# Kernel tuning notes

Hardware: AMD Instinct MI355X
Metric: run time of the kernel (lower is better)

## Reference

```python
import jax, jax.numpy as jnp
import numpy as np
import math

WINDOW = 2048
EMBED = 1024
BATCH = 8


def setup_inputs() -> dict:
    key = jax.random.key(0)
    ks = jax.random.split(key, 7)
    s = 1.0 / math.sqrt(EMBED)
    return {
        "embeddings": jax.random.normal(ks[0], (BATCH, WINDOW, EMBED), dtype=jnp.float32),
        "Wq": jax.random.uniform(ks[1], (EMBED, EMBED), jnp.float32, -s, s),
        "bq": jax.random.uniform(ks[2], (EMBED,), jnp.float32, -s, s),
        "Wk": jax.random.uniform(ks[3], (EMBED, EMBED), jnp.float32, -s, s),
        "bk": jax.random.uniform(ks[4], (EMBED,), jnp.float32, -s, s),
        "Wv": jax.random.uniform(ks[5], (EMBED, EMBED), jnp.float32, -s, s),
        "bv": jax.random.uniform(ks[6], (EMBED,), jnp.float32, -s, s),
    }


def reference(embeddings, Wq, bq, Wk, bk, Wv, bv):
    # Linear layers: x @ W.T + b (torch nn.Linear convention)
    Q = jnp.einsum('bse,fe->bsf', embeddings, Wq) + bq
    K = jnp.einsum('bse,fe->bsf', embeddings, Wk) + bk
    V = jnp.einsum('bse,fe->bsf', embeddings, Wv) + bv
    scale = 1.0 / math.sqrt(EMBED)
    # [B, S, S] score matrix: A[b, i, j] = Q_i . K_j / sqrt(d)
    A = jnp.einsum('bie,bje->bij', Q, K) * scale
    # causal additive mask: -inf where j > i (strictly upper triangular)
    mask = jnp.triu(jnp.full((WINDOW, WINDOW), -jnp.inf, dtype=A.dtype), k=1)
    A = A + mask
    # NOTE: faithful to original nn.Softmax(dim=1): normalize over QUERY axis
    P = jax.nn.softmax(A, axis=1)
    return jnp.einsum('bij,bje->bie', P, V)
```

## Files before the change

### kernel.cpp

```cpp
#include <hip/hip_runtime.h>
#include <stdint.h>

#define WINDOW 2048
#define EMBED  1024
#define BATCH  8
#define MTOT   (BATCH*WINDOW)

typedef unsigned short u16;
typedef __bf16 bf16x8 __attribute__((ext_vector_type(8)));
typedef float  f32x4  __attribute__((ext_vector_type(4)));

#define BK 64
#define KSCALE 0.04508422717564447f

#define BM2 256
#define BN2 256
#define HALF2 8192
#define PLD  260

#define AHALFR 4096
#define BHALFR 8192

#define WAITVM4 asm volatile("s_waitcnt vmcnt(4)" ::: "memory")
#define WAITVM3 asm volatile("s_waitcnt vmcnt(3)" ::: "memory")
#define WAITVM0 asm volatile("s_waitcnt vmcnt(0)" ::: "memory")
#define SBAR    __builtin_amdgcn_s_barrier()

__device__ __forceinline__ u16 f2bf(float f) {
  union { float f; unsigned u; } a; a.f = f;
  unsigned r = a.u + 0x7FFF + ((a.u >> 16) & 1);
  return (u16)(r >> 16);
}
__device__ __forceinline__ float bf2f(u16 u) {
  union { unsigned u; float f; } a; a.u = ((unsigned)u) << 16;
  return a.f;
}

__device__ __forceinline__ void gload16(const u16* g, u16* l) {
  __builtin_amdgcn_global_load_lds(
      (const __attribute__((address_space(1))) unsigned int*)g,
      (__attribute__((address_space(3))) unsigned int*)l, 16, 0, 0);
}


__device__ __forceinline__ void gemm256(
    const u16* __restrict__ A, int lda,
    const u16* __restrict__ B, int ldb,
    int nt, u16* lds, f32x4 acc[8][4])
{
  const int tid  = threadIdx.x;
  const int lane = tid & 63;
  const int wid  = tid >> 6;
  const int wm   = (wid >> 2) * 128;
  const int wn   = (wid & 3) * 64;
  const int lrow = lane & 15;
  const int hi   = lane >> 4;
  u16* dA = lds;
  u16* dB = lds + 4 * HALF2;

  int aoff[8], boff[4];
  #pragma unroll
  for (int mi = 0; mi < 8; ++mi) {
    int r = wm + mi * 16 + lrow;
    aoff[mi] = r * 32 + ((hi ^ ((r >> 1) & 3)) << 3);
  }
  #pragma unroll
  for (int ni = 0; ni < 4; ++ni) {
    int r = wn + ni * 16 + lrow;
    boff[ni] = r * 32 + ((hi ^ ((r >> 1) & 3)) << 3);
  }

  const int f0 = tid, f1 = 512 + tid;
  const int r0 = f0 >> 2, r1 = f1 >> 2;
  const int c0 = (((f0 & 3) ^ ((r0 >> 1) & 3)) << 3);
  const int c1 = (((f1 & 3) ^ ((r1 >> 1) & 3)) << 3);
  const u16* pA0 = A + (size_t)r0 * lda + c0;
  const u16* pA1 = A + (size_t)r1 * lda + c1;
  const u16* pB0 = B + (size_t)r0 * ldb + c0;
  const u16* pB1 = B + (size_t)r1 * ldb + c1;
  const int d0 = f0 * 8, d1 = f1 * 8;

  gload16(pA0,      dA + d0);         gload16(pA1,      dA + d1);
  gload16(pB0,      dB + d0);         gload16(pB1,      dB + d1);
  gload16(pA0 + 32, dA + HALF2 + d0); gload16(pA1 + 32, dA + HALF2 + d1);
  gload16(pB0 + 32, dB + HALF2 + d0); gload16(pB1 + 32, dB + HALF2 + d1);
  pA0 += BK; pA1 += BK; pB0 += BK; pB1 += BK;
  WAITVM4;
  SBAR;

  for (int t = 0; t < nt; ++t) {
    const int cb = (t & 1) * 2;
    const int nb = ((t + 1) & 1) * 2;
    u16* LA0 = dA + cb * HALF2;  u16* LA1 = LA0 + HALF2;
    u16* LB0 = dB + cb * HALF2;  u16* LB1 = LB0 + HALF2;
    const bool s = (t + 1) < nt;
    bf16x8 av[8], bv[4];

    #pragma unroll
    for (int mi = 0; mi < 8; ++mi) av[mi] = *(const bf16x8*)(LA0 + aoff[mi]);
    #pragma unroll
    for (int ni = 0; ni < 4; ++ni) bv[ni] = *(const bf16x8*)(LB0 + boff[ni]);
    if (s) {
      gload16(pA0, dA + nb * HALF2 + d0); gload16(pA1, dA + nb * HALF2 + d1);
      gload16(pB0, dB + nb * HALF2 + d0); gload16(pB1, dB + nb * HALF2 + d1);
    }
    __builtin_amdgcn_s_setprio(1);
    #pragma unroll
    for (int mi = 0; mi < 8; ++mi)
      #pragma unroll
      for (int ni = 0; ni < 4; ++ni)
        acc[mi][ni] = __builtin_amdgcn_mfma_f32_16x16x32_bf16(av[mi], bv[ni], acc[mi][ni], 0, 0, 0);
    __builtin_amdgcn_s_setprio(0);
    if (s) { WAITVM4; } else { WAITVM0; }
    SBAR;

    #pragma unroll
    for (int mi = 0; mi < 8; ++mi) av[mi] = *(const bf16x8*)(LA1 + aoff[mi]);
    #pragma unroll
    for (int ni = 0; ni < 4; ++ni) bv[ni] = *(const bf16x8*)(LB1 + boff[ni]);
    if (s) {
      gload16(pA0 + 32, dA + nb * HALF2 + HALF2 + d0); gload16(pA1 + 32, dA + nb * HALF2 + HALF2 + d1);
      gload16(pB0 + 32, dB + nb * HALF2 + HALF2 + d0); gload16(pB1 + 32, dB + nb * HALF2 + HALF2 + d1);
      pA0 += BK; pA1 += BK; pB0 += BK; pB1 += BK;
    }
    __builtin_amdgcn_s_setprio(1);
    #pragma unroll
    for (int mi = 0; mi < 8; ++mi)
      #pragma unroll
      for (int ni = 0; ni < 4; ++ni)
        acc[mi][ni] = __builtin_amdgcn_mfma_f32_16x16x32_bf16(av[mi], bv[ni], acc[mi][ni], 0, 0, 0);
    __builtin_amdgcn_s_setprio(0);
    if (s) { WAITVM4; }
    SBAR;
  }
}

__device__ __forceinline__ void gemm_rect(
    const u16* __restrict__ A, int lda,
    const u16* __restrict__ B, int ldb,
    int nt, u16* lds, f32x4 acc[4][4])
{
  const int tid  = threadIdx.x;
  const int lane = tid & 63;
  const int wid  = tid >> 6;
  const int wm   = (wid >> 2) * 64;
  const int wn   = (wid & 3) * 64;
  const int lrow = lane & 15;
  const int hi   = lane >> 4;
  u16* dA = lds;
  u16* dB = lds + 4 * AHALFR;

  int aoff[4], boff[4];
  #pragma unroll
  for (int mi = 0; mi < 4; ++mi) {
    int r = wm + mi * 16 + lrow;
    aoff[mi] = r * 32 + ((hi ^ ((r >> 1) & 3)) << 3);
  }
  #pragma unroll
  for (int ni = 0; ni < 4; ++ni) {
    int r = wn + ni * 16 + lrow;
    boff[ni] = r * 32 + ((hi ^ ((r >> 1) & 3)) << 3);
  }

  const int fa = tid;
  const int fb0 = tid, fb1 = 512 + tid;
  const int ra = fa >> 2, rb0 = fb0 >> 2, rb1 = fb1 >> 2;
  const int ca  = (((fa  & 3) ^ ((ra  >> 1) & 3)) << 3);
  const int cb0 = (((fb0 & 3) ^ ((rb0 >> 1) & 3)) << 3);
  const int cb1 = (((fb1 & 3) ^ ((rb1 >> 1) & 3)) << 3);
  const u16* pA  = A + (size_t)ra  * lda + ca;
  const u16* pB0 = B + (size_t)rb0 * ldb + cb0;
  const u16* pB1 = B + (size_t)rb1 * ldb + cb1;
  const int da = fa * 8, db0 = fb0 * 8, db1 = fb1 * 8;

  gload16(pA,       dA + da);
  gload16(pB0,      dB + db0);          gload16(pB1,      dB + db1);
  gload16(pA + 32,  dA + AHALFR + da);
  gload16(pB0 + 32, dB + BHALFR + db0); gload16(pB1 + 32, dB + BHALFR + db1);
  pA += BK; pB0 += BK; pB1 += BK;
  WAITVM3;
  SBAR;

  for (int t = 0; t < nt; ++t) {
    const int cb = (t & 1) * 2;
    const int nb = ((t + 1) & 1) * 2;
    u16* LA0 = dA + cb * AHALFR;  u16* LA1 = LA0 + AHALFR;
    u16* LB0 = dB + cb * BHALFR;  u16* LB1 = LB0 + BHALFR;
    const bool s = (t + 1) < nt;
    bf16x8 av[4], bv[4];

    #pragma unroll
    for (int mi = 0; mi < 4; ++mi) av[mi] = *(const bf16x8*)(LA0 + aoff[mi]);
    #pragma unroll
    for (int ni = 0; ni < 4; ++ni) bv[ni] = *(const bf16x8*)(LB0 + boff[ni]);
    if (s) {
      gload16(pA,  dA + nb * AHALFR + da);
      gload16(pB0, dB + nb * BHALFR + db0); gload16(pB1, dB + nb * BHALFR + db1);
    }
    __builtin_amdgcn_s_setprio(1);
    #pragma unroll
    for (int mi = 0; mi < 4; ++mi)
      #pragma unroll
      for (int ni = 0; ni < 4; ++ni)
        acc[mi][ni] = __builtin_amdgcn_mfma_f32_16x16x32_bf16(av[mi], bv[ni], acc[mi][ni], 0, 0, 0);
    __builtin_amdgcn_s_setprio(0);
    if (s) { WAITVM3; } else { WAITVM0; }
    SBAR;

    #pragma unroll
    for (int mi = 0; mi < 4; ++mi) av[mi] = *(const bf16x8*)(LA1 + aoff[mi]);
    #pragma unroll
    for (int ni = 0; ni < 4; ++ni) bv[ni] = *(const bf16x8*)(LB1 + boff[ni]);
    if (s) {
      gload16(pA + 32,  dA + nb * AHALFR + AHALFR + da);
      gload16(pB0 + 32, dB + nb * BHALFR + BHALFR + db0);
      gload16(pB1 + 32, dB + nb * BHALFR + BHALFR + db1);
      pA += BK; pB0 += BK; pB1 += BK;
    }
    __builtin_amdgcn_s_setprio(1);
    #pragma unroll
    for (int mi = 0; mi < 4; ++mi)
      #pragma unroll
      for (int ni = 0; ni < 4; ++ni)
        acc[mi][ni] = __builtin_amdgcn_mfma_f32_16x16x32_bf16(av[mi], bv[ni], acc[mi][ni], 0, 0, 0);
    __builtin_amdgcn_s_setprio(0);
    if (s) { WAITVM3; }
    SBAR;
  }
}

__global__ __launch_bounds__(256) void k_cvt(const float* __restrict__ in,
                                             u16* __restrict__ out, int n) {
  int i = (blockIdx.x * 256 + threadIdx.x) * 4;
  if (i >= n) return;
  float4 v = *(const float4*)(in + i);
  ushort4 o;
  o.x = f2bf(v.x); o.y = f2bf(v.y); o.z = f2bf(v.z); o.w = f2bf(v.w);
  *(ushort4*)(out + i) = o;
}

__global__ __launch_bounds__(256) void k_cvtw(const float* __restrict__ w0,
                                              const float* __restrict__ w1,
                                              const float* __restrict__ w2,
                                              u16* __restrict__ out) {
  const float* in = (blockIdx.y == 0) ? w0 : (blockIdx.y == 1) ? w1 : w2;
  u16* o = out + (size_t)blockIdx.y * EMBED * EMBED;
  int i = (blockIdx.x * 256 + threadIdx.x) * 4;
  float4 v = *(const float4*)(in + i);
  ushort4 r;
  r.x = f2bf(v.x); r.y = f2bf(v.y); r.z = f2bf(v.z); r.w = f2bf(v.w);
  *(ushort4*)(o + i) = r;
}

__global__ __launch_bounds__(512, 2) void k_qkv(
    const u16* __restrict__ Xb, const u16* __restrict__ Wb,
    const float* __restrict__ bq, const float* __restrict__ bk, const float* __restrict__ bv,
    u16* __restrict__ Q, u16* __restrict__ Ks, u16* __restrict__ V)
{
  __shared__ u16 lds[8 * HALF2];
  const int m0 = blockIdx.x * BM2;
  const int n0 = blockIdx.y * BN2;
  const int z  = blockIdx.z;
  const u16*   W    = Wb + (size_t)z * EMBED * EMBED;
  const float* bias = (z == 0) ? bq : (z == 1) ? bk : bv;
  u16* out          = (z == 0) ? Q  : (z == 1) ? Ks : V;
  const float scale = (z == 1) ? KSCALE : 1.0f;

  f32x4 acc[8][4];
  const f32x4 zz = {0.f,0.f,0.f,0.f};
  #pragma unroll
  for (int i = 0; i < 8; ++i) for (int j = 0; j < 4; ++j) acc[i][j] = zz;
  gemm256(Xb + (size_t)m0 * EMBED, EMBED, W + (size_t)n0 * EMBED, EMBED,
          EMBED / BK, lds, acc);

  const int lane = threadIdx.x & 63, wid = threadIdx.x >> 6;
  const int wm = (wid >> 2) * 128, wn = (wid & 3) * 64;
  const int lrow = lane & 15, hi = lane >> 4;
  #pragma unroll
  for (int mi = 0; mi < 8; ++mi)
    #pragma unroll
    for (int ni = 0; ni < 4; ++ni)
      #pragma unroll
      for (int rr = 0; rr < 4; ++rr) {
        int gm = m0 + wm + mi * 16 + hi * 4 + rr;
        int gn = n0 + wn + ni * 16 + lrow;
        out[(size_t)gm * EMBED + gn] = f2bf((acc[mi][ni][rr] + bias[gn]) * scale);
      }
}

__global__ __launch_bounds__(512, 2) void k_spd(
    const u16* __restrict__ Q, const u16* __restrict__ Ks,
    u16* __restrict__ P, float* __restrict__ D)
{
  __shared__ u16 lds[BM2 * PLD];
  const int sblk = blockIdx.x;

  if (sblk < 256) {
    const int xcd = sblk & 7;
    const int q   = sblk >> 3;
    int it = 0;
    while (q >= ((it + 1) * (it + 2)) / 2) ++it;
    const int jt = q - (it * (it + 1)) / 2;
    const int b  = (xcd - it) & 7;
    const int i0 = it * BM2;
    const int j0 = jt * BN2;

    const u16* A = Q  + (size_t)b * WINDOW * EMBED + (size_t)i0 * EMBED;
    const u16* B = Ks + (size_t)b * WINDOW * EMBED + (size_t)j0 * EMBED;
    f32x4 acc[8][4];
    const f32x4 zz = {0.f,0.f,0.f,0.f};
    #pragma unroll
    for (int i = 0; i < 8; ++i) for (int j = 0; j < 4; ++j) acc[i][j] = zz;
    gemm256(A, EMBED, B, EMBED, EMBED / BK, lds, acc);

    u16* Pb   = P + (size_t)b * WINDOW * WINDOW;
    float* Db = D + (size_t)b * WINDOW;
    const int tid  = threadIdx.x;
    const int lane = tid & 63, wid = tid >> 6;
    const int wm = (wid >> 2) * 128, wn = (wid & 3) * 64;
    const int lrow = lane & 15, hi = lane >> 4;

    #pragma unroll
    for (int ni = 0; ni < 4; ++ni) {
      int lj = wn + ni * 16 + lrow;
      float csum = 0.f;
      #pragma unroll
      for (int mi = 0; mi < 8; ++mi)
        #pragma unroll
        for (int rr = 0; rr < 4; ++rr) {
          int li = wm + mi * 16 + hi * 4 + rr;
          float p = ((i0 + li) >= (j0 + lj)) ? exp2f(acc[mi][ni][rr]) : 0.0f;
          lds[li * PLD + lj] = f2bf(p);
          csum += p;
        }
      csum += __shfl_xor(csum, 16, 64);
      csum += __shfl_xor(csum, 32, 64);
      if (hi == 0) atomicAdd(&Db[j0 + lj], csum);
    }
    __syncthreads();

    #pragma unroll
    for (int it2 = 0; it2 < 16; ++it2) {
      int f   = it2 * 512 + tid;
      int row = f >> 5;
      int c   = f & 31;
      bf16x8 v = *(const bf16x8*)(lds + row * PLD + c * 8);
      *(bf16x8*)(Pb + (size_t)(i0 + row) * WINDOW + j0 + c * 8) = v;
    }
  } else {
    const int ih   = sblk - 256;
    const int xcd  = ih & 7;
    const int h    = ih >> 3;
    const int jt   = 4 + (h >> 1);
    const int half = h & 1;
    const int it   = 7;
    const int b    = (xcd - it) & 7;
    const int i0   = it * BM2 + half * 128;
    const int j0   = jt * BN2;

    const u16* A = Q  + (size_t)b * WINDOW * EMBED + (size_t)i0 * EMBED;
    const u16* B = Ks + (size_t)b * WINDOW * EMBED + (size_t)j0 * EMBED;
    f32x4 acc[4][4];
    const f32x4 zz = {0.f,0.f,0.f,0.f};
    #pragma unroll
    for (int i = 0; i < 4; ++i) for (int j = 0; j < 4; ++j) acc[i][j] = zz;
    gemm_rect(A, EMBED, B, EMBED, EMBED / BK, lds, acc);

    u16* Pb   = P + (size_t)b * WINDOW * WINDOW;
    float* Db = D + (size_t)b * WINDOW;
    const int lane = threadIdx.x & 63, wid = threadIdx.x >> 6;
    const int wm = (wid >> 2) * 64, wn = (wid & 3) * 64;
    const int lrow = lane & 15, hi = lane >> 4;
    #pragma unroll
    for (int ni = 0; ni < 4; ++ni) {
      int gj = j0 + wn + ni * 16 + lrow;
      float csum = 0.f;
      #pragma unroll
      for (int mi = 0; mi < 4; ++mi)
        #pragma unroll
        for (int rr = 0; rr < 4; ++rr) {
          int gi = i0 + wm + mi * 16 + hi * 4 + rr;
          float p = (gi >= gj) ? exp2f(acc[mi][ni][rr]) : 0.0f;
          Pb[(size_t)gi * WINDOW + gj] = f2bf(p);
          csum += p;
        }
      csum += __shfl_xor(csum, 16, 64);
      csum += __shfl_xor(csum, 32, 64);
      if (hi == 0) atomicAdd(&Db[gj], csum);
    }
  }
}

__global__ __launch_bounds__(256) void k_vdt(
    const u16* __restrict__ V, const float* __restrict__ D, u16* __restrict__ Vdt)
{
  __shared__ u16 tile[64][68];
  const int j0 = blockIdx.x * 64, e0 = blockIdx.y * 64, b = blockIdx.z;
  const u16* Vb = V   + (size_t)b * WINDOW * EMBED;
  u16* Tb       = Vdt + (size_t)b * EMBED * WINDOW;
  const float* Db = D + (size_t)b * WINDOW;
  const int t = threadIdx.x;
  const int rr = t >> 4;
  const int cc = (t & 15) * 4;
  #pragma unroll
  for (int p = 0; p < 4; ++p) {
    int r = p * 16 + rr;
    *(uint2*)&tile[r][cc] = *(const uint2*)(Vb + (size_t)(j0 + r) * EMBED + e0 + cc);
  }
  __syncthreads();
  #pragma unroll
  for (int p = 0; p < 4; ++p) {
    int er = p * 16 + rr;
    ushort4 o;
    o.x = f2bf(bf2f(tile[cc + 0][er]) / Db[j0 + cc + 0]);
    o.y = f2bf(bf2f(tile[cc + 1][er]) / Db[j0 + cc + 1]);
    o.z = f2bf(bf2f(tile[cc + 2][er]) / Db[j0 + cc + 2]);
    o.w = f2bf(bf2f(tile[cc + 3][er]) / Db[j0 + cc + 3]);
    *(ushort4*)(Tb + (size_t)(e0 + er) * WINDOW + j0 + cc) = o;
  }
}

__global__ __launch_bounds__(512, 2) void k_out(
    const u16* __restrict__ P, const u16* __restrict__ Vdt, float* __restrict__ O)
{
  __shared__ u16 lds[8 * HALF2];
  const int s   = blockIdx.x;
  const int xcd = s & 7;
  const int q   = s >> 3;
  const int et  = q & 3;
  const int it  = 7 - (q >> 2);
  const int b   = (xcd - it) & 7;
  const int i0  = it * BM2;
  const int e0  = et * BN2;

  const u16* A = P   + (size_t)b * WINDOW * WINDOW + (size_t)i0 * WINDOW;
  const u16* B = Vdt + (size_t)b * EMBED * WINDOW  + (size_t)e0 * WINDOW;
  f32x4 acc[8][4];
  const f32x4 zz = {0.f,0.f,0.f,0.f};
  #pragma unroll
  for (int i = 0; i < 8; ++i) for (int j = 0; j < 4; ++j) acc[i][j] = zz;
  gemm256(A, WINDOW, B, WINDOW, (i0 + BM2) / BK, lds, acc);

  float* Ob = O + (size_t)b * WINDOW * EMBED;
  const int lane = threadIdx.x & 63, wid = threadIdx.x >> 6;
  const int wm = (wid >> 2) * 128, wn = (wid & 3) * 64;
  const int lrow = lane & 15, hi = lane >> 4;
  #pragma unroll
  for (int mi = 0; mi < 8; ++mi)
    #pragma unroll
    for (int ni = 0; ni < 4; ++ni)
      #pragma unroll
      for (int rr = 0; rr < 4; ++rr) {
        int gi = i0 + wm + mi * 16 + hi * 4 + rr;
        int ge = e0 + wn + ni * 16 + lrow;
        Ob[(size_t)gi * EMBED + ge] = acc[mi][ni][rr];
      }
}

extern "C" void kernel_launch(void* const* d_in, const int* in_sizes, int n_in,
                              void* d_out, int out_size, void* d_ws, size_t ws_size,
                              hipStream_t stream) {
  const float* X  = (const float*)d_in[0];
  const float* Wq = (const float*)d_in[1];
  const float* bq = (const float*)d_in[2];
  const float* Wk = (const float*)d_in[3];
  const float* bk = (const float*)d_in[4];
  const float* Wv = (const float*)d_in[5];
  const float* bv = (const float*)d_in[6];
  float* O = (float*)d_out;

  char* ws = (char*)d_ws;
  size_t off = 0;
  auto alloc = [&](size_t bytes) -> void* {
    void* p = ws + off; off += (bytes + 255) & ~(size_t)255; return p;
  };
  u16*  Xb  = (u16*)alloc((size_t)MTOT * EMBED * 2);
  u16*  Wb  = (u16*)alloc((size_t)3 * EMBED * EMBED * 2);
  u16*  Qb  = (u16*)alloc((size_t)MTOT * EMBED * 2);
  u16*  Kb  = (u16*)alloc((size_t)MTOT * EMBED * 2);
  u16*  Vb  = (u16*)alloc((size_t)MTOT * EMBED * 2);
  u16*  Vdt = (u16*)alloc((size_t)BATCH * EMBED * WINDOW * 2);
  u16*  P   = (u16*)alloc((size_t)BATCH * WINDOW * WINDOW * 2);
  float* D  = (float*)alloc((size_t)MTOT * 4);
  (void)ws_size; (void)in_sizes; (void)n_in; (void)out_size;

  k_cvt<<<dim3((MTOT * EMBED / 4 + 255) / 256), 256, 0, stream>>>(X, Xb, MTOT * EMBED);
  k_cvtw<<<dim3(EMBED * EMBED / 4 / 256, 3), 256, 0, stream>>>(Wq, Wk, Wv, Wb);

  k_qkv<<<dim3(MTOT / BM2, EMBED / BN2, 3), 512, 0, stream>>>(Xb, Wb, bq, bk, bv, Qb, Kb, Vb);

  (void)hipMemsetAsync(D, 0, (size_t)MTOT * 4, stream);
  k_spd<<<dim3(320), 512, 0, stream>>>(Qb, Kb, P, D);

  k_vdt<<<dim3(WINDOW / 64, EMBED / 64, BATCH), 256, 0, stream>>>(Vb, D, Vdt);

  k_out<<<dim3(256), 512, 0, stream>>>(P, Vdt, O);
}
```

Baseline: 273.6 us.

## Split long causal row tiles in final GEMM across two blocks with atomic reduction

The P·V output GEMM has triangular work: row tiles near the bottom need many more K iterations than those near the top. This change splits the four heaviest row tiles (it 4–7) into two K halves, each done by a separate block, and combines the halves with atomicAdd into an output region that is zeroed beforehand. The grid grows from 256 to 384 blocks to even out load across the 256 CUs. The cost is extra memset launches, float atomic traffic on half the output, and a non-deterministic summation order.

After: 313.3 us. +14.5%, slower.

```diff
diff --git a/kernel.cpp b/kernel.cpp
--- a/kernel.cpp
+++ b/kernel.cpp
@@ -427,34 +427,58 @@
   const int s   = blockIdx.x;
   const int xcd = s & 7;
   const int q   = s >> 3;
-  const int et  = q & 3;
-  const int it  = 7 - (q >> 2);
-  const int b   = (xcd - it) & 7;
-  const int i0  = it * BM2;
-  const int e0  = et * BN2;
-
-  const u16* A = P   + (size_t)b * WINDOW * WINDOW + (size_t)i0 * WINDOW;
-  const u16* B = Vdt + (size_t)b * EMBED * WINDOW  + (size_t)e0 * WINDOW;
+  int it, et, kh = -1;
+  if      (q <  8) { it = 7; kh = (q >> 2) & 1;        et = q & 3;        }
+  else if (q < 12) { it = 3;                           et = q - 8;        }
+  else if (q < 20) { it = 6; kh = ((q - 12) >> 2) & 1; et = (q - 12) & 3; }
+  else if (q < 28) { it = 5; kh = ((q - 20) >> 2) & 1; et = (q - 20) & 3; }
+  else if (q < 32) { it = 2;                           et = q - 28;       }
+  else if (q < 40) { it = 4; kh = ((q - 32) >> 2) & 1; et = (q - 32) & 3; }
+  else if (q < 44) { it = 1;                           et = q - 40;       }
+  else             { it = 0;                           et = q - 44;       }
+
+  const int b  = (xcd - it) & 7;
+  const int i0 = it * BM2;
+  const int e0 = et * BN2;
+  const int ntfull = 4 * (it + 1);
+  const int nt     = (kh < 0) ? ntfull : ntfull / 2;
+  const int kstart = (kh <= 0) ? 0 : nt;
+
+  const u16* A = P   + (size_t)b * WINDOW * WINDOW + (size_t)i0 * WINDOW + (size_t)kstart * BK;
+  const u16* B = Vdt + (size_t)b * EMBED * WINDOW  + (size_t)e0 * WINDOW + (size_t)kstart * BK;
   f32x4 acc[8][4];
   const f32x4 zz = {0.f,0.f,0.f,0.f};
   #pragma unroll
   for (int i = 0; i < 8; ++i) for (int j = 0; j < 4; ++j) acc[i][j] = zz;
-  gemm256(A, WINDOW, B, WINDOW, (i0 + BM2) / BK, lds, acc);
+  gemm256(A, WINDOW, B, WINDOW, nt, lds, acc);
 
   float* Ob = O + (size_t)b * WINDOW * EMBED;
   const int lane = threadIdx.x & 63, wid = threadIdx.x >> 6;
   const int wm = (wid >> 2) * 128, wn = (wid & 3) * 64;
   const int lrow = lane & 15, hi = lane >> 4;
-  #pragma unroll
-  for (int mi = 0; mi < 8; ++mi)
-    #pragma unroll
-    for (int ni = 0; ni < 4; ++ni)
-      #pragma unroll
-      for (int rr = 0; rr < 4; ++rr) {
-        int gi = i0 + wm + mi * 16 + hi * 4 + rr;
-        int ge = e0 + wn + ni * 16 + lrow;
-        Ob[(size_t)gi * EMBED + ge] = acc[mi][ni][rr];
-      }
+  if (kh < 0) {
+    #pragma unroll
+    for (int mi = 0; mi < 8; ++mi)
+      #pragma unroll
+      for (int ni = 0; ni < 4; ++ni)
+        #pragma unroll
+        for (int rr = 0; rr < 4; ++rr) {
+          int gi = i0 + wm + mi * 16 + hi * 4 + rr;
+          int ge = e0 + wn + ni * 16 + lrow;
+          Ob[(size_t)gi * EMBED + ge] = acc[mi][ni][rr];
+        }
+  } else {
+    #pragma unroll
+    for (int mi = 0; mi < 8; ++mi)
+      #pragma unroll
+      for (int ni = 0; ni < 4; ++ni)
+        #pragma unroll
+        for (int rr = 0; rr < 4; ++rr) {
+          int gi = i0 + wm + mi * 16 + hi * 4 + rr;
+          int ge = e0 + wn + ni * 16 + lrow;
+          atomicAdd(&Ob[(size_t)gi * EMBED + ge], acc[mi][ni][rr]);
+        }
+  }
 }
 
 extern "C" void kernel_launch(void* const* d_in, const int* in_sizes, int n_in,
@@ -493,6 +517,9 @@
   k_spd<<<dim3(320), 512, 0, stream>>>(Qb, Kb, P, D);
 
   k_vdt<<<dim3(WINDOW / 64, EMBED / 64, BATCH), 256, 0, stream>>>(Vb, D, Vdt);
-
-  k_out<<<dim3(256), 512, 0, stream>>>(P, Vdt, O);
-}
+  for (int b = 0; b < BATCH; ++b)
+    (void)hipMemsetAsync(O + ((size_t)b * WINDOW + 1024) * EMBED, 0,
+                         (size_t)1024 * EMBED * 4, stream);
+
+  k_out<<<dim3(384), 512, 0, stream>>>(P, Vdt, O);
+}
```

## Split heavy causal row tiles of the output GEMM into half-height blocks

Applied to the files above, without the earlier changes.

The P·V output kernel gets a new work split. Row tiles in the upper half of the causal triangle, which carry the most K-steps, become two 128-row blocks each, and each half uses its own trimmed K extent. Lighter row tiles keep the original 256-row blocks. The launch grows from 256 to 384 blocks. The aim is to shrink the long tail caused by uneven triangular work, at the cost of smaller tiles with less reuse for the split part.

Result: no change. 270.0 us (median of 2 runs) (-1.3%).

```diff
diff --git a/kernel.cpp b/kernel.cpp
--- a/kernel.cpp
+++ b/kernel.cpp
@@ -427,34 +427,69 @@
   const int s   = blockIdx.x;
   const int xcd = s & 7;
   const int q   = s >> 3;
-  const int et  = q & 3;
-  const int it  = 7 - (q >> 2);
-  const int b   = (xcd - it) & 7;
-  const int i0  = it * BM2;
-  const int e0  = et * BN2;
-
-  const u16* A = P   + (size_t)b * WINDOW * WINDOW + (size_t)i0 * WINDOW;
-  const u16* B = Vdt + (size_t)b * EMBED * WINDOW  + (size_t)e0 * WINDOW;
-  f32x4 acc[8][4];
-  const f32x4 zz = {0.f,0.f,0.f,0.f};
-  #pragma unroll
-  for (int i = 0; i < 8; ++i) for (int j = 0; j < 4; ++j) acc[i][j] = zz;
-  gemm256(A, WINDOW, B, WINDOW, (i0 + BM2) / BK, lds, acc);
-
-  float* Ob = O + (size_t)b * WINDOW * EMBED;
+  float* ObBase;
   const int lane = threadIdx.x & 63, wid = threadIdx.x >> 6;
-  const int wm = (wid >> 2) * 128, wn = (wid & 3) * 64;
   const int lrow = lane & 15, hi = lane >> 4;
-  #pragma unroll
-  for (int mi = 0; mi < 8; ++mi)
-    #pragma unroll
-    for (int ni = 0; ni < 4; ++ni)
-      #pragma unroll
-      for (int rr = 0; rr < 4; ++rr) {
-        int gi = i0 + wm + mi * 16 + hi * 4 + rr;
-        int ge = e0 + wn + ni * 16 + lrow;
-        Ob[(size_t)gi * EMBED + ge] = acc[mi][ni][rr];
-      }
+
+  if (q < 32) {
+    const int it  = 7 - (q >> 3);
+    const int sub = q & 7;
+    const int hb  = sub >> 2;
+    const int et  = sub & 3;
+    const int b   = (xcd - it) & 7;
+    const int i0  = it * BM2 + (hb ? 0 : 128);
+    const int e0  = et * BN2;
+    const int nt  = hb ? (4 * it + 2) : (4 * it + 4);
+
+    const u16* A = P   + (size_t)b * WINDOW * WINDOW + (size_t)i0 * WINDOW;
+    const u16* B = Vdt + (size_t)b * EMBED * WINDOW  + (size_t)e0 * WINDOW;
+    f32x4 acc[4][4];
+    const f32x4 zz = {0.f,0.f,0.f,0.f};
+    #pragma unroll
+    for (int i = 0; i < 4; ++i) for (int j = 0; j < 4; ++j) acc[i][j] = zz;
+    gemm_rect(A, WINDOW, B, WINDOW, nt, lds, acc);
+
+    ObBase = O + (size_t)b * WINDOW * EMBED;
+    const int wm = (wid >> 2) * 64, wn = (wid & 3) * 64;
+    #pragma unroll
+    for (int mi = 0; mi < 4; ++mi)
+      #pragma unroll
+      for (int ni = 0; ni < 4; ++ni)
+        #pragma unroll
+        for (int rr = 0; rr < 4; ++rr) {
+          int gi = i0 + wm + mi * 16 + hi * 4 + rr;
+          int ge = e0 + wn + ni * 16 + lrow;
+          ObBase[(size_t)gi * EMBED + ge] = acc[mi][ni][rr];
+        }
+  } else {
+    const int qq = q - 32;
+    const int it = 3 - (qq >> 2);
+    const int et = qq & 3;
+    const int b  = (xcd - it) & 7;
+    const int i0 = it * BM2;
+    const int e0 = et * BN2;
+
+    const u16* A = P   + (size_t)b * WINDOW * WINDOW + (size_t)i0 * WINDOW;
+    const u16* B = Vdt + (size_t)b * EMBED * WINDOW  + (size_t)e0 * WINDOW;
+    f32x4 acc[8][4];
+    const f32x4 zz = {0.f,0.f,0.f,0.f};
+    #pragma unroll
+    for (int i = 0; i < 8; ++i) for (int j = 0; j < 4; ++j) acc[i][j] = zz;
+    gemm256(A, WINDOW, B, WINDOW, 4 * (it + 1), lds, acc);
+
+    ObBase = O + (size_t)b * WINDOW * EMBED;
+    const int wm = (wid >> 2) * 128, wn = (wid & 3) * 64;
+    #pragma unroll
+    for (int mi = 0; mi < 8; ++mi)
+      #pragma unroll
+      for (int ni = 0; ni < 4; ++ni)
+        #pragma unroll
+        for (int rr = 0; rr < 4; ++rr) {
+          int gi = i0 + wm + mi * 16 + hi * 4 + rr;
+          int ge = e0 + wn + ni * 16 + lrow;
+          ObBase[(size_t)gi * EMBED + ge] = acc[mi][ni][rr];
+        }
+  }
 }
 
 extern "C" void kernel_launch(void* const* d_in, const int* in_sizes, int n_in,
@@ -494,5 +529,5 @@
 
   k_vdt<<<dim3(WINDOW / 64, EMBED / 64, BATCH), 256, 0, stream>>>(Vb, D, Vdt);
 
-  k_out<<<dim3(256), 512, 0, stream>>>(P, Vdt, O);
-}
+  k_out<<<dim3(384), 512, 0, stream>>>(P, Vdt, O);
+}
```
